# Performance work log

Hardware: AMD Instinct MI355X
Metric: run time of the kernel (lower is better)

Reference implementation:

```python
import jax, jax.numpy as jnp
import numpy as np

NEG = -1e9
THRESH = 0.97


def _gat(x, emask, W, al, ar, b):
    # x: [B,N,Fin], emask: [B,N,N] bool (src,dst), W: [Fin,H*D], al/ar: [H,D], b: [H*D]
    B, N, _ = x.shape
    H, D = al.shape
    feat = (x @ W).reshape(B, N, H, D)
    el = jnp.einsum('bnhd,hd->bnh', feat, al)
    er = jnp.einsum('bnhd,hd->bnh', feat, ar)
    # DGL GATConv: e = leaky_relu(el[src] + er[dst]); edge softmax over incoming edges of dst
    e = jax.nn.leaky_relu(el[:, :, None, :] + er[:, None, :, :], 0.2)  # [B,src,dst,H]
    e = jnp.where(emask[..., None], e, NEG)
    a = jnp.where(emask[..., None], jax.nn.softmax(e, axis=1), 0.0)  # softmax over src
    rst = jnp.einsum('bsdh,bshf->bdhf', a, feat).reshape(B, N, H * D)
    return jax.nn.elu(rst + b)


def _sem_attention(z, nmask, W1, b1, W2):
    # z: [B,N,M,Dz]; masked mean over all valid nodes of the batched graph (== DGL batch semantics)
    p = jnp.tanh(z @ W1 + b1) @ W2  # [B,N,M,1]
    w = (p * nmask[:, :, None, None]).sum(axis=(0, 1)) / nmask.sum()  # [M,1]
    beta = jax.nn.softmax(w, axis=0)  # [M,1]
    return (beta[None, None] * z).sum(axis=2)  # [B,N,Dz]


def _han_layer(h, emasks, nmask, fc, al, ar, b, sW1, sb1, sW2):
    M = fc.shape[0]
    embs = [_gat(h, emasks[m], fc[m], al[m], ar[m], b[m]) for m in range(M)]
    z = jnp.stack(embs, axis=2)  # [B,N,M,H*D]
    return _sem_attention(z, nmask, sW1, sb1, sW2)


def setup_inputs() -> dict:
    key = jax.random.key(0)
    ks = jax.random.split(key, 24)
    B, M, N, Fin = 4, 5, 1000, 64
    H, D = 4, 64
    HD = H * D  # 256
    SH = 128    # semantic attention hidden
    OUT = 5
    s = 0.1
    inp = {
        'x': jax.random.normal(ks[0], (B, M, N, Fin), dtype=jnp.float32),
        'adj': jax.random.uniform(ks[1], (B, M, N, N), dtype=jnp.float32),
        'node_nums': jax.random.randint(ks[2], (B,), 0, N),
        # layer 1 (in = Fin)
        'gat_fc1': jax.random.normal(ks[3], (M, Fin, HD), dtype=jnp.float32) * s,
        'gat_al1': jax.random.normal(ks[4], (M, H, D), dtype=jnp.float32) * s,
        'gat_ar1': jax.random.normal(ks[5], (M, H, D), dtype=jnp.float32) * s,
        'gat_b1': jnp.zeros((M, HD), dtype=jnp.float32),
        'sem_W1_1': jax.random.normal(ks[6], (HD, SH), dtype=jnp.float32) * s,
        'sem_b1_1': jnp.zeros((SH,), dtype=jnp.float32),
        'sem_W2_1': jax.random.normal(ks[7], (SH, 1), dtype=jnp.float32) * s,
        # layer 2 (in = HD)
        'gat_fc2': jax.random.normal(ks[8], (M, HD, HD), dtype=jnp.float32) * s,
        'gat_al2': jax.random.normal(ks[9], (M, H, D), dtype=jnp.float32) * s,
        'gat_ar2': jax.random.normal(ks[10], (M, H, D), dtype=jnp.float32) * s,
        'gat_b2': jnp.zeros((M, HD), dtype=jnp.float32),
        'sem_W1_2': jax.random.normal(ks[11], (HD, SH), dtype=jnp.float32) * s,
        'sem_b1_2': jnp.zeros((SH,), dtype=jnp.float32),
        'sem_W2_2': jax.random.normal(ks[12], (SH, 1), dtype=jnp.float32) * s,
        # prediction head
        'pred_W': jax.random.normal(ks[13], (HD, OUT), dtype=jnp.float32) * s,
        'pred_b': jnp.zeros((OUT,), dtype=jnp.float32),
    }
    return inp


def reference(x, adj, node_nums, gat_fc1, gat_al1, gat_ar1, gat_b1,
              sem_W1_1, sem_b1_1, sem_W2_1,
              gat_fc2, gat_al2, gat_ar2, gat_b2,
              sem_W1_2, sem_b1_2, sem_W2_2,
              pred_W, pred_b):
    B, M, N, Fin = x.shape
    h = x[:, 0]  # original cat-then-[0]: only channel-0 features are used
    nmask = (jnp.arange(N)[None, :] < node_nums[:, None]).astype(x.dtype)  # [B,N]
    pair = (nmask[:, :, None] * nmask[:, None, :]) > 0  # [B,N,N]
    emasks = [(adj[:, m] > THRESH) & pair for m in range(M)]
    h = _han_layer(h, emasks, nmask, gat_fc1, gat_al1, gat_ar1, gat_b1,
                   sem_W1_1, sem_b1_1, sem_W2_1)
    h = _han_layer(h, emasks, nmask, gat_fc2, gat_al2, gat_ar2, gat_b2,
                   sem_W1_2, sem_b1_2, sem_W2_2)
    logits = (h @ pred_W + pred_b) * nmask[:, :, None]  # scatter into padded [B,N,OUT]
    return logits
```

## Files before the change

kernel.cpp:

```cpp
#include <hip/hip_runtime.h>
#include <hip/hip_bf16.h>

#define B_ 4
#define M_ 5
#define N_ 1000
#define FIN 64
#define H_ 4
#define D_ 64
#define HD 256
#define SH 128
#define OUTD 5
#define NW 16
#define THRESH_ 0.97f

typedef unsigned short u16;
typedef u16 us8 __attribute__((ext_vector_type(8)));
typedef short s16x8 __attribute__((ext_vector_type(8)));
typedef float f32x4 __attribute__((ext_vector_type(4)));

__device__ inline u16 bf16_bits(float v) {
  __hip_bfloat16 h = __float2bfloat16(v);
  return *reinterpret_cast<u16*>(&h);
}
__device__ inline float bf16_val(u16 b) {
  __hip_bfloat16 h;
  *reinterpret_cast<u16*>(&h) = b;
  return __bfloat162float(h);
}
__device__ inline float b2f(u16 u) {
  union { unsigned int i; float f; } c;
  c.i = ((unsigned int)u) << 16;
  return c.f;
}
__device__ inline void split2(float v, u16& h, u16& l) {
  h = bf16_bits(v);
  l = bf16_bits(v - bf16_val(h));
}
__device__ inline void beta_from_sums(const float* __restrict__ psum,
                                      const int* __restrict__ node_nums,
                                      float* bb) {
  float tot = (float)(node_nums[0] + node_nums[1] + node_nums[2] + node_nums[3]);
  float w[M_], mx = -1e30f;
#pragma unroll
  for (int m = 0; m < M_; ++m) {
    w[m] = psum[m] / tot;
    mx = fmaxf(mx, w[m]);
  }
  float s = 0.f;
#pragma unroll
  for (int m = 0; m < M_; ++m) {
    w[m] = __expf(w[m] - mx);
    s += w[m];
  }
  float inv = 1.f / s;
#pragma unroll
  for (int m = 0; m < M_; ++m) bb[m] = w[m] * inv;
}

__device__ void splitT_body(const float* __restrict__ s, u16* __restrict__ hiT,
                            u16* __restrict__ loT, int K, int N, int k0, int n0,
                            char* smem) {
  float(*tile)[33] = (float(*)[33])smem;
  int tid = threadIdx.x;
  int kl = tid >> 3, nq = (tid & 7) * 4;
  *(float4*)&tile[kl][nq] = *(const float4*)(s + (size_t)(k0 + kl) * N + n0 + nq);
  __syncthreads();
  int nl = tid >> 3, kq = (tid & 7) * 4;
  ushort4 h, l;
  split2(tile[kq + 0][nl], h.x, l.x);
  split2(tile[kq + 1][nl], h.y, l.y);
  split2(tile[kq + 2][nl], h.z, l.z);
  split2(tile[kq + 3][nl], h.w, l.w);
  size_t o = (size_t)(n0 + nl) * K + k0 + kq;
  *(ushort4*)(hiT + o) = h;
  *(ushort4*)(loT + o) = l;
}

__global__ __launch_bounds__(256) void prep_all(
    const float* __restrict__ adj, const int* __restrict__ node_nums,
    unsigned long long* __restrict__ maskW,
    const float* __restrict__ fc1, u16* __restrict__ fc1Th, u16* __restrict__ fc1Tl,
    const float* __restrict__ fc2, u16* __restrict__ fc2Th, u16* __restrict__ fc2Tl,
    const float* __restrict__ sW1_1, u16* __restrict__ sW1Th1, u16* __restrict__ sW1Tl1,
    const float* __restrict__ sW1_2, u16* __restrict__ sW1Th2, u16* __restrict__ sW1Tl2) {
  __shared__ __align__(16) char smem[4608];
  int bi = blockIdx.x;
  int tid = threadIdx.x;
  if (bi < 5120) {
    int bx = bi & 15, by = (bi >> 4) & 15, bm = bi >> 8;
    int b = bm / M_;
    int s0 = bx * 64, d0 = by * 64;
    int nn = node_nums[b];
    unsigned char(*tile)[65] = (unsigned char(*)[65])smem;
    const float* arow = adj + (size_t)bm * N_ * N_;
#pragma unroll
    for (int k = 0; k < 16; ++k) {
      int idx = k * 256 + tid;
      int sl = idx >> 6, dl = idx & 63;
      int s = s0 + sl, d = d0 + dl;
      unsigned char v = 0;
      if (s < nn && d < nn && s < N_ && d < N_)
        v = (arow[(size_t)s * N_ + d] > THRESH_) ? 1 : 0;
      tile[sl][dl] = v;
    }
    __syncthreads();
    int w = tid >> 6, lane = tid & 63;
#pragma unroll
    for (int j = 0; j < 16; ++j) {
      int dl = w * 16 + j;
      bool act = tile[lane][dl] != 0;
      unsigned long long word = __ballot(act);
      int d = d0 + dl;
      if (lane == 0 && d < N_)
        maskW[((size_t)bm * N_ + d) * NW + bx] = word;
    }
    return;
  }
  bi -= 5120;
  if (bi < 80) {
    int kx = bi % 2, ny = (bi / 2) % 8, z = bi / 16;
    splitT_body(fc1 + (size_t)z * FIN * HD, fc1Th + (size_t)z * HD * FIN,
                fc1Tl + (size_t)z * HD * FIN, FIN, HD, kx * 32, ny * 32, smem);
    return;
  }
  bi -= 80;
  if (bi < 320) {
    int kx = bi % 8, ny = (bi / 8) % 8, z = bi / 64;
    splitT_body(fc2 + (size_t)z * HD * HD, fc2Th + (size_t)z * HD * HD,
                fc2Tl + (size_t)z * HD * HD, HD, HD, kx * 32, ny * 32, smem);
    return;
  }
  bi -= 320;
  if (bi < 32) {
    int kx = bi % 8, ny = bi / 8;
    splitT_body(sW1_1, sW1Th1, sW1Tl1, HD, SH, kx * 32, ny * 32, smem);
    return;
  }
  bi -= 32;
  {
    int kx = bi % 8, ny = bi / 8;
    splitT_body(sW1_2, sW1Th2, sW1Tl2, HD, SH, kx * 32, ny * 32, smem);
  }
}

__global__ __launch_bounds__(256) void gemm_mfma3(
    const float* __restrict__ A, int Mz, size_t aZ,
    const u16* __restrict__ Bh, const u16* __restrict__ Bl, size_t bZ,
    u16* __restrict__ Cbf, size_t cZ,
    int Mrows, int K, int Nc,
    const float* __restrict__ al, const float* __restrict__ ar,
    float* __restrict__ el, float* __restrict__ er) {
  __shared__ u16 sAh[64][40], sAl[64][40], sBh[64][40], sBl[64][40];
  __shared__ float elbuf[64][2], erbuf[64][2];
  int z = blockIdx.z;
  int b = z / Mz, m = z % Mz;
  const float* Ab = A + (size_t)b * aZ;
  const u16* Bhb = Bh + (size_t)m * bZ;
  const u16* Blb = Bl + (size_t)m * bZ;
  u16* Cfb = Cbf + (size_t)z * cZ;
  int row0 = blockIdx.x * 64, col0 = blockIdx.y * 64;
  int tid = threadIdx.x;
  int arow = tid >> 2, akq = (tid & 3) * 8;
  int wid = tid >> 6, lane = tid & 63;
  int wr = (wid >> 1) * 32, wc = (wid & 1) * 32;
  int lrow = lane & 15, kseg = (lane >> 4) * 8;
  f32x4 zero4 = {0.f, 0.f, 0.f, 0.f};
  f32x4 acc[2][2];
  acc[0][0] = zero4; acc[0][1] = zero4; acc[1][0] = zero4; acc[1][1] = zero4;
  for (int k0 = 0; k0 < K; k0 += 32) {
    float4 a0 = make_float4(0.f, 0.f, 0.f, 0.f), a1 = a0;
    int gr = row0 + arow;
    if (gr < Mrows) {
      const float* ap = Ab + (size_t)gr * K + k0 + akq;
      a0 = *(const float4*)ap;
      a1 = *(const float4*)(ap + 4);
    }
    us8 hv, lv;
    {
      u16 th, tl;
      split2(a0.x, th, tl); hv[0] = th; lv[0] = tl;
      split2(a0.y, th, tl); hv[1] = th; lv[1] = tl;
      split2(a0.z, th, tl); hv[2] = th; lv[2] = tl;
      split2(a0.w, th, tl); hv[3] = th; lv[3] = tl;
      split2(a1.x, th, tl); hv[4] = th; lv[4] = tl;
      split2(a1.y, th, tl); hv[5] = th; lv[5] = tl;
      split2(a1.z, th, tl); hv[6] = th; lv[6] = tl;
      split2(a1.w, th, tl); hv[7] = th; lv[7] = tl;
    }
    *(us8*)&sAh[arow][akq] = hv;
    *(us8*)&sAl[arow][akq] = lv;
    us8 bv = *(const us8*)(Bhb + (size_t)(col0 + arow) * K + k0 + akq);
    us8 blv = *(const us8*)(Blb + (size_t)(col0 + arow) * K + k0 + akq);
    *(us8*)&sBh[arow][akq] = bv;
    *(us8*)&sBl[arow][akq] = blv;
    __syncthreads();
    s16x8 aH[2], aL[2], bH[2], bL[2];
#pragma unroll
    for (int i = 0; i < 2; ++i) {
      aH[i] = *(const s16x8*)&sAh[wr + 16 * i + lrow][kseg];
      aL[i] = *(const s16x8*)&sAl[wr + 16 * i + lrow][kseg];
      bH[i] = *(const s16x8*)&sBh[wc + 16 * i + lrow][kseg];
      bL[i] = *(const s16x8*)&sBl[wc + 16 * i + lrow][kseg];
    }
#pragma unroll
    for (int i = 0; i < 2; ++i)
#pragma unroll
      for (int j = 0; j < 2; ++j) {
        acc[i][j] = __builtin_amdgcn_mfma_f32_16x16x32_bf16(aH[i], bH[j], acc[i][j], 0, 0, 0);
        acc[i][j] = __builtin_amdgcn_mfma_f32_16x16x32_bf16(aH[i], bL[j], acc[i][j], 0, 0, 0);
        acc[i][j] = __builtin_amdgcn_mfma_f32_16x16x32_bf16(aL[i], bH[j], acc[i][j], 0, 0, 0);
      }
    __syncthreads();
  }
#pragma unroll
  for (int i = 0; i < 2; ++i)
#pragma unroll
    for (int j = 0; j < 2; ++j) {
      int ccol = col0 + wc + 16 * j + lrow;
#pragma unroll
      for (int r = 0; r < 4; ++r) {
        int crow = row0 + wr + 16 * i + (lane >> 4) * 4 + r;
        if (crow < Mrows)
          Cfb[(size_t)crow * Nc + ccol] = bf16_bits(acc[i][j][r]);
      }
    }
  float alv0 = al[m * HD + col0 + wc + lrow];
  float alv1 = al[m * HD + col0 + wc + 16 + lrow];
  float arv0 = ar[m * HD + col0 + wc + lrow];
  float arv1 = ar[m * HD + col0 + wc + 16 + lrow];
#pragma unroll
  for (int i = 0; i < 2; ++i)
#pragma unroll
    for (int r = 0; r < 4; ++r) {
      float pl = acc[i][0][r] * alv0 + acc[i][1][r] * alv1;
      float pr = acc[i][0][r] * arv0 + acc[i][1][r] * arv1;
#pragma unroll
      for (int s = 1; s < 16; s <<= 1) {
        pl += __shfl_xor(pl, s, 64);
        pr += __shfl_xor(pr, s, 64);
      }
      if (lrow == 0) {
        int rl = wr + 16 * i + (lane >> 4) * 4 + r;
        elbuf[rl][wc >> 5] = pl;
        erbuf[rl][wc >> 5] = pr;
      }
    }
  __syncthreads();
  if (tid < 64) {
    int grow = row0 + tid;
    if (grow < Mrows) {
      int h = col0 >> 6;
      size_t bmN = (size_t)(b * M_ + m) * N_;
      el[(bmN + grow) * H_ + h] = elbuf[tid][0] + elbuf[tid][1];
      er[(bmN + grow) * H_ + h] = erbuf[tid][0] + erbuf[tid][1];
    }
  }
}

__global__ __launch_bounds__(256) void gat_agg(
    const unsigned long long* __restrict__ maskW, const u16* __restrict__ featbf,
    const float* __restrict__ el, const float* __restrict__ er,
    const float* __restrict__ gb, u16* __restrict__ zbh,
    float* __restrict__ psum) {
  int wid = threadIdx.x >> 6, lane = threadIdx.x & 63;
  const int NWGQ = (B_ * M_ * N_ / 4) / 8;
  int orig = blockIdx.x;
  if (orig == 0 && threadIdx.x < 8) psum[threadIdx.x] = 0.f;
  int bid = (orig & 7) * NWGQ + (orig >> 3);
  int gw = bid * 4 + wid;
  int d = gw % N_, bm = gw / N_;
  int m = bm % M_, b = bm / M_;
  __shared__ u16 slist_all[4][1032];
  u16* slist = slist_all[wid];

  const unsigned long long* mrow = maskW + ((size_t)bm * N_ + d) * NW;
  int cnt = 0;
#pragma unroll
  for (int q = 0; q < NW / 2; ++q) {
    ulonglong2 wp = *(const ulonglong2*)(mrow + q * 2);
    unsigned long long w0 = wp.x, w1 = wp.y;
    if (w0) {
      if ((w0 >> lane) & 1ull) {
        int pos = cnt + (int)__popcll(w0 & ((1ull << lane) - 1ull));
        slist[pos] = (u16)(q * 128 + lane);
      }
      cnt += (int)__popcll(w0);
    }
    if (w1) {
      if ((w1 >> lane) & 1ull) {
        int pos = cnt + (int)__popcll(w1 & ((1ull << lane) - 1ull));
        slist[pos] = (u16)(q * 128 + 64 + lane);
      }
      cnt += (int)__popcll(w1);
    }
  }

  int h = lane >> 4;
  float4 bias4 = *(const float4*)(gb + m * HD + lane * 4);
  size_t zoff = ((size_t)(b * N_ + d) * M_ + m) * HD + lane * 4;
  float4 o;
  if (cnt == 0) {
    o.x = bias4.x > 0.f ? bias4.x : (__expf(bias4.x) - 1.f);
    o.y = bias4.y > 0.f ? bias4.y : (__expf(bias4.y) - 1.f);
    o.z = bias4.z > 0.f ? bias4.z : (__expf(bias4.z) - 1.f);
    o.w = bias4.w > 0.f ? bias4.w : (__expf(bias4.w) - 1.f);
  } else {
    if (lane < 4) slist[cnt + lane] = slist[0];
    size_t bmN = (size_t)bm * N_;
    float erv = er[(bmN + d) * H_ + h];
    const float* elb = el + bmN * H_;
    const u16* fbb = featbf + bmN * HD;
    int lane4 = lane * 4;
    float den0 = 0.f, den1 = 0.f, den2 = 0.f, den3 = 0.f;
    f32x4 A0 = {0.f, 0.f, 0.f, 0.f}, A1 = A0, A2 = A0, A3 = A0;
    for (int i = 0; i < cnt; i += 4) {
      ushort4 s4 = *(const ushort4*)&slist[i];
      float e0 = elb[(size_t)s4.x * H_ + h];
      float e1 = elb[(size_t)s4.y * H_ + h];
      float e2 = elb[(size_t)s4.z * H_ + h];
      float e3 = elb[(size_t)s4.w * H_ + h];
      ushort4 g0 = *(const ushort4*)(fbb + (size_t)s4.x * HD + lane4);
      ushort4 g1 = *(const ushort4*)(fbb + (size_t)s4.y * HD + lane4);
      ushort4 g2 = *(const ushort4*)(fbb + (size_t)s4.z * HD + lane4);
      ushort4 g3 = *(const ushort4*)(fbb + (size_t)s4.w * HD + lane4);
      float v0 = e0 + erv; v0 = v0 > 0.f ? v0 : 0.2f * v0;
      float v1 = e1 + erv; v1 = v1 > 0.f ? v1 : 0.2f * v1;
      float v2 = e2 + erv; v2 = v2 > 0.f ? v2 : 0.2f * v2;
      float v3 = e3 + erv; v3 = v3 > 0.f ? v3 : 0.2f * v3;
      float w0 = __expf(v0);
      float w1 = __expf(v1) * ((i + 1 < cnt) ? 1.f : 0.f);
      float w2 = __expf(v2) * ((i + 2 < cnt) ? 1.f : 0.f);
      float w3 = __expf(v3) * ((i + 3 < cnt) ? 1.f : 0.f);
      f32x4 f0 = {b2f(g0.x), b2f(g0.y), b2f(g0.z), b2f(g0.w)};
      f32x4 f1 = {b2f(g1.x), b2f(g1.y), b2f(g1.z), b2f(g1.w)};
      f32x4 f2 = {b2f(g2.x), b2f(g2.y), b2f(g2.z), b2f(g2.w)};
      f32x4 f3 = {b2f(g3.x), b2f(g3.y), b2f(g3.z), b2f(g3.w)};
      den0 += w0; den1 += w1; den2 += w2; den3 += w3;
      A0 += w0 * f0; A1 += w1 * f1; A2 += w2 * f2; A3 += w3 * f3;
    }
    float den = (den0 + den1) + (den2 + den3);
    f32x4 A = (A0 + A1) + (A2 + A3);
    float inv = 1.f / den;
    o.x = A[0] * inv + bias4.x;
    o.y = A[1] * inv + bias4.y;
    o.z = A[2] * inv + bias4.z;
    o.w = A[3] * inv + bias4.w;
    o.x = o.x > 0.f ? o.x : (__expf(o.x) - 1.f);
    o.y = o.y > 0.f ? o.y : (__expf(o.y) - 1.f);
    o.z = o.z > 0.f ? o.z : (__expf(o.z) - 1.f);
    o.w = o.w > 0.f ? o.w : (__expf(o.w) - 1.f);
  }
  ushort4 hh;
  hh.x = bf16_bits(o.x);
  hh.y = bf16_bits(o.y);
  hh.z = bf16_bits(o.z);
  hh.w = bf16_bits(o.w);
  *(ushort4*)(zbh + zoff) = hh;
}

__global__ __launch_bounds__(256) void gemm_sem(
    const u16* __restrict__ Ah, const u16* __restrict__ Bh,
    const float* __restrict__ bias, const float* __restrict__ W2,
    float* __restrict__ psum, const int* __restrict__ node_nums, int Mrows) {
  __shared__ u16 sA[64][40], sB[64][40];
  __shared__ float redm[M_];
  int row0 = blockIdx.x * 64, col0 = blockIdx.y * 64;
  int tid = threadIdx.x;
  int arow = tid >> 2, akq = (tid & 3) * 8;
  int wid = tid >> 6, lane = tid & 63;
  int wr = (wid >> 1) * 32, wc = (wid & 1) * 32;
  int lrow = lane & 15, kseg = (lane >> 4) * 8;
  if (tid < M_) redm[tid] = 0.f;
  f32x4 zero4 = {0.f, 0.f, 0.f, 0.f};
  f32x4 acc[2][2];
  acc[0][0] = zero4; acc[0][1] = zero4; acc[1][0] = zero4; acc[1][1] = zero4;
  for (int k0 = 0; k0 < HD; k0 += 32) {
    us8 av = {0, 0, 0, 0, 0, 0, 0, 0};
    int gr = row0 + arow;
    if (gr < Mrows) av = *(const us8*)(Ah + (size_t)gr * HD + k0 + akq);
    *(us8*)&sA[arow][akq] = av;
    us8 bv = *(const us8*)(Bh + (size_t)(col0 + arow) * HD + k0 + akq);
    *(us8*)&sB[arow][akq] = bv;
    __syncthreads();
    s16x8 aH[2], bH[2];
#pragma unroll
    for (int i = 0; i < 2; ++i) {
      aH[i] = *(const s16x8*)&sA[wr + 16 * i + lrow][kseg];
      bH[i] = *(const s16x8*)&sB[wc + 16 * i + lrow][kseg];
    }
#pragma unroll
    for (int i = 0; i < 2; ++i)
#pragma unroll
      for (int j = 0; j < 2; ++j)
        acc[i][j] = __builtin_amdgcn_mfma_f32_16x16x32_bf16(aH[i], bH[j], acc[i][j], 0, 0, 0);
    __syncthreads();
  }
  int nn0 = node_nums[0], nn1 = node_nums[1], nn2 = node_nums[2], nn3 = node_nums[3];
#pragma unroll
  for (int i = 0; i < 2; ++i) {
#pragma unroll
    for (int r = 0; r < 4; ++r) {
      float part = 0.f;
#pragma unroll
      for (int j = 0; j < 2; ++j) {
        int ccol = col0 + wc + 16 * j + lrow;
        float v = tanhf(acc[i][j][r] + bias[ccol]);
        part += v * W2[ccol];
      }
#pragma unroll
      for (int s = 1; s < 16; s <<= 1) part += __shfl_xor(part, s, 64);
      int crow = row0 + wr + 16 * i + (lane >> 4) * 4 + r;
      if (lrow == 0 && crow < Mrows) {
        int m = crow % M_;
        int bn = crow / M_;
        int bb = bn / N_, n = bn % N_;
        int nn = (bb == 0) ? nn0 : (bb == 1) ? nn1 : (bb == 2) ? nn2 : nn3;
        if (n < nn) atomicAdd(&redm[m], part);
      }
    }
  }
  __syncthreads();
  if (tid < M_) atomicAdd(&psum[tid], redm[tid]);
}

__global__ __launch_bounds__(256) void sem_combine(const u16* __restrict__ zbh,
                                                   const float* __restrict__ psum,
                                                   const int* __restrict__ node_nums,
                                                   float* __restrict__ hout) {
  float bb[M_];
  beta_from_sums(psum, node_nums, bb);
  int q = blockIdx.x * 256 + threadIdx.x;
  int hd4 = (q & 63) * 4;
  int bn = q >> 6;
  const u16* zr = zbh + (size_t)bn * M_ * HD + hd4;
  f32x4 acc = {0.f, 0.f, 0.f, 0.f};
#pragma unroll
  for (int m = 0; m < M_; ++m) {
    ushort4 g = *(const ushort4*)(zr + m * HD);
    f32x4 f = {b2f(g.x), b2f(g.y), b2f(g.z), b2f(g.w)};
    acc += bb[m] * f;
  }
  *(f32x4*)(hout + (size_t)bn * HD + hd4) = acc;
}

__global__ __launch_bounds__(256) void sem_combine_pred(
    const u16* __restrict__ zbh, const float* __restrict__ psum,
    const int* __restrict__ node_nums, const float* __restrict__ W,
    const float* __restrict__ bias, float* __restrict__ out) {
  float bb[M_];
  beta_from_sums(psum, node_nums, bb);
  int row = blockIdx.x * 4 + (threadIdx.x >> 6);
  int lane = threadIdx.x & 63;
  int b = row / N_, n = row % N_;
  const u16* zr = zbh + (size_t)row * M_ * HD + lane * 4;
  float hx = 0.f, hy = 0.f, hz = 0.f, hw = 0.f;
#pragma unroll
  for (int m = 0; m < M_; ++m) {
    ushort4 g = *(const ushort4*)(zr + m * HD);
    hx += bb[m] * b2f(g.x);
    hy += bb[m] * b2f(g.y);
    hz += bb[m] * b2f(g.z);
    hw += bb[m] * b2f(g.w);
  }
  int k = lane * 4;
  float res[OUTD];
#pragma unroll
  for (int o = 0; o < OUTD; ++o) {
    float v = hx * W[(k + 0) * OUTD + o] + hy * W[(k + 1) * OUTD + o] +
              hz * W[(k + 2) * OUTD + o] + hw * W[(k + 3) * OUTD + o];
#pragma unroll
    for (int s = 1; s < 64; s <<= 1) v += __shfl_xor(v, s, 64);
    res[o] = v;
  }
  if (lane == 0) {
    float nm = (n < node_nums[b]) ? 1.f : 0.f;
#pragma unroll
    for (int o = 0; o < OUTD; ++o)
      out[(size_t)row * OUTD + o] = (res[o] + bias[o]) * nm;
  }
}

extern "C" void kernel_launch(void* const* d_in, const int* in_sizes, int n_in,
                              void* d_out, int out_size, void* d_ws, size_t ws_size,
                              hipStream_t stream) {
  const float* x = (const float*)d_in[0];
  const float* adj = (const float*)d_in[1];
  const int* node_nums = (const int*)d_in[2];
  const float* fc1 = (const float*)d_in[3];
  const float* al1 = (const float*)d_in[4];
  const float* ar1 = (const float*)d_in[5];
  const float* gb1 = (const float*)d_in[6];
  const float* sW1_1 = (const float*)d_in[7];
  const float* sb1_1 = (const float*)d_in[8];
  const float* sW2_1 = (const float*)d_in[9];
  const float* fc2 = (const float*)d_in[10];
  const float* al2 = (const float*)d_in[11];
  const float* ar2 = (const float*)d_in[12];
  const float* gb2 = (const float*)d_in[13];
  const float* sW1_2 = (const float*)d_in[14];
  const float* sb1_2 = (const float*)d_in[15];
  const float* sW2_2 = (const float*)d_in[16];
  const float* predW = (const float*)d_in[17];
  const float* predb = (const float*)d_in[18];
  float* out = (float*)d_out;

  char* ws = (char*)d_ws;
  size_t off = 0;
  unsigned long long* maskW = (unsigned long long*)(ws + off);
  off += (size_t)B_ * M_ * N_ * NW * 8;
  u16* featbf = (u16*)(ws + off); off += (size_t)B_ * M_ * N_ * HD * 2;
  float* el = (float*)(ws + off); off += (size_t)B_ * M_ * N_ * H_ * 4;
  float* er = (float*)(ws + off); off += (size_t)B_ * M_ * N_ * H_ * 4;
  u16* zbh = (u16*)(ws + off); off += (size_t)B_ * N_ * M_ * HD * 2;
  float* h1 = (float*)(ws + off); off += (size_t)B_ * N_ * HD * 4;
  float* psum = (float*)(ws + off); off += 64;
  u16* fc1Th = (u16*)(ws + off); off += (size_t)M_ * HD * FIN * 2;
  u16* fc1Tl = (u16*)(ws + off); off += (size_t)M_ * HD * FIN * 2;
  u16* fc2Th = (u16*)(ws + off); off += (size_t)M_ * HD * HD * 2;
  u16* fc2Tl = (u16*)(ws + off); off += (size_t)M_ * HD * HD * 2;
  u16* sW1Th1 = (u16*)(ws + off); off += (size_t)SH * HD * 2;
  u16* sW1Tl1 = (u16*)(ws + off); off += (size_t)SH * HD * 2;
  u16* sW1Th2 = (u16*)(ws + off); off += (size_t)SH * HD * 2;
  u16* sW1Tl2 = (u16*)(ws + off); off += (size_t)SH * HD * 2;

  const int ROWS = B_ * N_ * M_;
  const int PREP_BLOCKS = 5120 + 80 + 320 + 32 + 32;

  prep_all<<<dim3(PREP_BLOCKS), 256, 0, stream>>>(
      adj, node_nums, maskW, fc1, fc1Th, fc1Tl, fc2, fc2Th, fc2Tl,
      sW1_1, sW1Th1, sW1Tl1, sW1_2, sW1Th2, sW1Tl2);

  gemm_mfma3<<<dim3(16, HD / 64, B_ * M_), 256, 0, stream>>>(
      x, M_, (size_t)M_ * N_ * FIN, fc1Th, fc1Tl, (size_t)HD * FIN,
      featbf, (size_t)N_ * HD, N_, FIN, HD, al1, ar1, el, er);
  gat_agg<<<dim3(ROWS / 4), 256, 0, stream>>>(maskW, featbf, el, er, gb1, zbh, psum);
  gemm_sem<<<dim3((ROWS + 63) / 64, SH / 64), 256, 0, stream>>>(
      zbh, sW1Th1, sb1_1, sW2_1, psum, node_nums, ROWS);
  sem_combine<<<dim3(B_ * N_ * HD / 1024), 256, 0, stream>>>(zbh, psum, node_nums, h1);

  gemm_mfma3<<<dim3(16, HD / 64, B_ * M_), 256, 0, stream>>>(
      h1, M_, (size_t)N_ * HD, fc2Th, fc2Tl, (size_t)HD * HD,
      featbf, (size_t)N_ * HD, N_, HD, HD, al2, ar2, el, er);
  gat_agg<<<dim3(ROWS / 4), 256, 0, stream>>>(maskW, featbf, el, er, gb2, zbh, psum);
  gemm_sem<<<dim3((ROWS + 63) / 64, SH / 64), 256, 0, stream>>>(
      zbh, sW1Th2, sb1_2, sW2_2, psum, node_nums, ROWS);
  sem_combine_pred<<<dim3(B_ * N_ / 4), 256, 0, stream>>>(
      zbh, psum, node_nums, predW, predb, out);
}
```

Measured before the change: 164.6 us.

## Fuse semantic combine into layer-2 GEMM and process two destinations per wave

Drops the separate sem_combine kernel and the h1 buffer. The layer-2 feature GEMM now builds its A operand on the fly as the beta-weighted sum of the five bf16 metapath embeddings. gat_agg is restructured so each wave aggregates two destination nodes (d and d+500) together with interleaved gathers, halving the grid and adding memory-level parallelism. In exchange, the GEMM redoes the beta-weighted sum for every column block, and the paired destinations pad to the longer of their two neighbor lists.

New measurement: 192.0 us. 16.6% more time.

```diff
diff --git a/kernel.cpp b/kernel.cpp
--- a/kernel.cpp
+++ b/kernel.cpp
@@ -145,6 +145,8 @@
 
 __global__ __launch_bounds__(256) void gemm_mfma3(
     const float* __restrict__ A, int Mz, size_t aZ,
+    const u16* __restrict__ zsrc, const float* __restrict__ psum,
+    const int* __restrict__ node_nums,
     const u16* __restrict__ Bh, const u16* __restrict__ Bl, size_t bZ,
     u16* __restrict__ Cbf, size_t cZ,
     int Mrows, int K, int Nc,
@@ -154,7 +156,7 @@
   __shared__ float elbuf[64][2], erbuf[64][2];
   int z = blockIdx.z;
   int b = z / Mz, m = z % Mz;
-  const float* Ab = A + (size_t)b * aZ;
+  const float* Ab = A ? (A + (size_t)b * aZ) : nullptr;
   const u16* Bhb = Bh + (size_t)m * bZ;
   const u16* Blb = Bl + (size_t)m * bZ;
   u16* Cfb = Cbf + (size_t)z * cZ;
@@ -164,28 +166,41 @@
   int wid = tid >> 6, lane = tid & 63;
   int wr = (wid >> 1) * 32, wc = (wid & 1) * 32;
   int lrow = lane & 15, kseg = (lane >> 4) * 8;
+  float bbw[M_];
+  if (zsrc) beta_from_sums(psum, node_nums, bbw);
   f32x4 zero4 = {0.f, 0.f, 0.f, 0.f};
   f32x4 acc[2][2];
   acc[0][0] = zero4; acc[0][1] = zero4; acc[1][0] = zero4; acc[1][1] = zero4;
   for (int k0 = 0; k0 < K; k0 += 32) {
-    float4 a0 = make_float4(0.f, 0.f, 0.f, 0.f), a1 = a0;
+    float a8[8];
+#pragma unroll
+    for (int e = 0; e < 8; ++e) a8[e] = 0.f;
     int gr = row0 + arow;
     if (gr < Mrows) {
-      const float* ap = Ab + (size_t)gr * K + k0 + akq;
-      a0 = *(const float4*)ap;
-      a1 = *(const float4*)(ap + 4);
+      if (zsrc) {
+        const u16* zr = zsrc + ((size_t)(b * N_ + gr) * M_) * HD + k0 + akq;
+#pragma unroll
+        for (int mm = 0; mm < M_; ++mm) {
+          us8 g = *(const us8*)(zr + mm * HD);
+#pragma unroll
+          for (int e = 0; e < 8; ++e) a8[e] += bbw[mm] * b2f(g[e]);
+        }
+      } else {
+        const float* ap = Ab + (size_t)gr * K + k0 + akq;
+        float4 q0 = *(const float4*)ap;
+        float4 q1 = *(const float4*)(ap + 4);
+        a8[0] = q0.x; a8[1] = q0.y; a8[2] = q0.z; a8[3] = q0.w;
+        a8[4] = q1.x; a8[5] = q1.y; a8[6] = q1.z; a8[7] = q1.w;
+      }
     }
     us8 hv, lv;
     {
       u16 th, tl;
-      split2(a0.x, th, tl); hv[0] = th; lv[0] = tl;
-      split2(a0.y, th, tl); hv[1] = th; lv[1] = tl;
-      split2(a0.z, th, tl); hv[2] = th; lv[2] = tl;
-      split2(a0.w, th, tl); hv[3] = th; lv[3] = tl;
-      split2(a1.x, th, tl); hv[4] = th; lv[4] = tl;
-      split2(a1.y, th, tl); hv[5] = th; lv[5] = tl;
-      split2(a1.z, th, tl); hv[6] = th; lv[6] = tl;
-      split2(a1.w, th, tl); hv[7] = th; lv[7] = tl;
+#pragma unroll
+      for (int e = 0; e < 8; ++e) {
+        split2(a8[e], th, tl);
+        hv[e] = th; lv[e] = tl;
+      }
     }
     *(us8*)&sAh[arow][akq] = hv;
     *(us8*)&sAl[arow][akq] = lv;
@@ -263,99 +278,143 @@
     const float* __restrict__ gb, u16* __restrict__ zbh,
     float* __restrict__ psum) {
   int wid = threadIdx.x >> 6, lane = threadIdx.x & 63;
-  const int NWGQ = (B_ * M_ * N_ / 4) / 8;
+  const int NWG = (B_ * M_ * 500) / 4;
   int orig = blockIdx.x;
   if (orig == 0 && threadIdx.x < 8) psum[threadIdx.x] = 0.f;
-  int bid = (orig & 7) * NWGQ + (orig >> 3);
-  int gw = bid * 4 + wid;
-  int d = gw % N_, bm = gw / N_;
+  int q = NWG >> 3, r = NWG & 7;
+  int xcd = orig & 7, ii = orig >> 3;
+  int bid = (xcd < r ? xcd * (q + 1) : r * (q + 1) + (xcd - r) * q) + ii;
+  int ghw = bid * 4 + wid;
+  int bm = ghw / 500;
+  int db = ghw % 500;
+  int d0 = db, d1 = db + 500;
   int m = bm % M_, b = bm / M_;
-  __shared__ u16 slist_all[4][1032];
-  u16* slist = slist_all[wid];
-
-  const unsigned long long* mrow = maskW + ((size_t)bm * N_ + d) * NW;
-  int cnt = 0;
-#pragma unroll
-  for (int q = 0; q < NW / 2; ++q) {
-    ulonglong2 wp = *(const ulonglong2*)(mrow + q * 2);
-    unsigned long long w0 = wp.x, w1 = wp.y;
-    if (w0) {
-      if ((w0 >> lane) & 1ull) {
-        int pos = cnt + (int)__popcll(w0 & ((1ull << lane) - 1ull));
-        slist[pos] = (u16)(q * 128 + lane);
-      }
-      cnt += (int)__popcll(w0);
-    }
-    if (w1) {
-      if ((w1 >> lane) & 1ull) {
-        int pos = cnt + (int)__popcll(w1 & ((1ull << lane) - 1ull));
-        slist[pos] = (u16)(q * 128 + 64 + lane);
-      }
-      cnt += (int)__popcll(w1);
-    }
-  }
+  __shared__ u16 slist_all[4][2][1040];
+  u16* sl0 = slist_all[wid][0];
+  u16* sl1 = slist_all[wid][1];
+  if (lane < 4) { sl0[lane] = 0; sl1[lane] = 0; }
+
+  const unsigned long long* mr0 = maskW + ((size_t)bm * N_ + d0) * NW;
+  const unsigned long long* mr1 = maskW + ((size_t)bm * N_ + d1) * NW;
+  unsigned long long lm = (1ull << lane) - 1ull;
+  int c0 = 0, c1 = 0;
+#pragma unroll
+  for (int qq = 0; qq < NW / 2; ++qq) {
+    ulonglong2 wp0 = *(const ulonglong2*)(mr0 + qq * 2);
+    ulonglong2 wp1 = *(const ulonglong2*)(mr1 + qq * 2);
+    unsigned long long w00 = wp0.x, w01 = wp0.y, w10 = wp1.x, w11 = wp1.y;
+    if (w00) {
+      if ((w00 >> lane) & 1ull) sl0[c0 + (int)__popcll(w00 & lm)] = (u16)(qq * 128 + lane);
+      c0 += (int)__popcll(w00);
+    }
+    if (w01) {
+      if ((w01 >> lane) & 1ull) sl0[c0 + (int)__popcll(w01 & lm)] = (u16)(qq * 128 + 64 + lane);
+      c0 += (int)__popcll(w01);
+    }
+    if (w10) {
+      if ((w10 >> lane) & 1ull) sl1[c1 + (int)__popcll(w10 & lm)] = (u16)(qq * 128 + lane);
+      c1 += (int)__popcll(w10);
+    }
+    if (w11) {
+      if ((w11 >> lane) & 1ull) sl1[c1 + (int)__popcll(w11 & lm)] = (u16)(qq * 128 + 64 + lane);
+      c1 += (int)__popcll(w11);
+    }
+  }
+  int cmax = ((c0 > c1 ? c0 : c1) + 3) & ~3;
+  u16 p0 = sl0[0], p1 = sl1[0];
+  for (int t = c0 + lane; t < cmax; t += 64) sl0[t] = p0;
+  for (int t = c1 + lane; t < cmax; t += 64) sl1[t] = p1;
 
   int h = lane >> 4;
-  float4 bias4 = *(const float4*)(gb + m * HD + lane * 4);
-  size_t zoff = ((size_t)(b * N_ + d) * M_ + m) * HD + lane * 4;
-  float4 o;
-  if (cnt == 0) {
-    o.x = bias4.x > 0.f ? bias4.x : (__expf(bias4.x) - 1.f);
-    o.y = bias4.y > 0.f ? bias4.y : (__expf(bias4.y) - 1.f);
-    o.z = bias4.z > 0.f ? bias4.z : (__expf(bias4.z) - 1.f);
-    o.w = bias4.w > 0.f ? bias4.w : (__expf(bias4.w) - 1.f);
-  } else {
-    if (lane < 4) slist[cnt + lane] = slist[0];
-    size_t bmN = (size_t)bm * N_;
-    float erv = er[(bmN + d) * H_ + h];
-    const float* elb = el + bmN * H_;
-    const u16* fbb = featbf + bmN * HD;
-    int lane4 = lane * 4;
-    float den0 = 0.f, den1 = 0.f, den2 = 0.f, den3 = 0.f;
-    f32x4 A0 = {0.f, 0.f, 0.f, 0.f}, A1 = A0, A2 = A0, A3 = A0;
-    for (int i = 0; i < cnt; i += 4) {
-      ushort4 s4 = *(const ushort4*)&slist[i];
-      float e0 = elb[(size_t)s4.x * H_ + h];
-      float e1 = elb[(size_t)s4.y * H_ + h];
-      float e2 = elb[(size_t)s4.z * H_ + h];
-      float e3 = elb[(size_t)s4.w * H_ + h];
-      ushort4 g0 = *(const ushort4*)(fbb + (size_t)s4.x * HD + lane4);
-      ushort4 g1 = *(const ushort4*)(fbb + (size_t)s4.y * HD + lane4);
-      ushort4 g2 = *(const ushort4*)(fbb + (size_t)s4.z * HD + lane4);
-      ushort4 g3 = *(const ushort4*)(fbb + (size_t)s4.w * HD + lane4);
-      float v0 = e0 + erv; v0 = v0 > 0.f ? v0 : 0.2f * v0;
-      float v1 = e1 + erv; v1 = v1 > 0.f ? v1 : 0.2f * v1;
-      float v2 = e2 + erv; v2 = v2 > 0.f ? v2 : 0.2f * v2;
-      float v3 = e3 + erv; v3 = v3 > 0.f ? v3 : 0.2f * v3;
-      float w0 = __expf(v0);
-      float w1 = __expf(v1) * ((i + 1 < cnt) ? 1.f : 0.f);
-      float w2 = __expf(v2) * ((i + 2 < cnt) ? 1.f : 0.f);
-      float w3 = __expf(v3) * ((i + 3 < cnt) ? 1.f : 0.f);
-      f32x4 f0 = {b2f(g0.x), b2f(g0.y), b2f(g0.z), b2f(g0.w)};
-      f32x4 f1 = {b2f(g1.x), b2f(g1.y), b2f(g1.z), b2f(g1.w)};
-      f32x4 f2 = {b2f(g2.x), b2f(g2.y), b2f(g2.z), b2f(g2.w)};
-      f32x4 f3 = {b2f(g3.x), b2f(g3.y), b2f(g3.z), b2f(g3.w)};
-      den0 += w0; den1 += w1; den2 += w2; den3 += w3;
-      A0 += w0 * f0; A1 += w1 * f1; A2 += w2 * f2; A3 += w3 * f3;
-    }
-    float den = (den0 + den1) + (den2 + den3);
-    f32x4 A = (A0 + A1) + (A2 + A3);
-    float inv = 1.f / den;
-    o.x = A[0] * inv + bias4.x;
-    o.y = A[1] * inv + bias4.y;
-    o.z = A[2] * inv + bias4.z;
-    o.w = A[3] * inv + bias4.w;
-    o.x = o.x > 0.f ? o.x : (__expf(o.x) - 1.f);
-    o.y = o.y > 0.f ? o.y : (__expf(o.y) - 1.f);
-    o.z = o.z > 0.f ? o.z : (__expf(o.z) - 1.f);
-    o.w = o.w > 0.f ? o.w : (__expf(o.w) - 1.f);
-  }
-  ushort4 hh;
-  hh.x = bf16_bits(o.x);
-  hh.y = bf16_bits(o.y);
-  hh.z = bf16_bits(o.z);
-  hh.w = bf16_bits(o.w);
-  *(ushort4*)(zbh + zoff) = hh;
+  int lane4 = lane * 4;
+  float4 bias4 = *(const float4*)(gb + m * HD + lane4);
+  size_t bmN = (size_t)bm * N_;
+  float erv0 = er[(bmN + d0) * H_ + h];
+  float erv1 = er[(bmN + d1) * H_ + h];
+  const float* elb = el + bmN * H_;
+  const u16* fbb = featbf + bmN * HD;
+
+  float dA0 = 0.f, dA1 = 0.f, dA2 = 0.f, dA3 = 0.f;
+  float dB0 = 0.f, dB1 = 0.f, dB2 = 0.f, dB3 = 0.f;
+  f32x4 zz = {0.f, 0.f, 0.f, 0.f};
+  f32x4 AA0 = zz, AA1 = zz, AA2 = zz, AA3 = zz;
+  f32x4 BB0 = zz, BB1 = zz, BB2 = zz, BB3 = zz;
+  for (int i = 0; i < cmax; i += 4) {
+    ushort4 sa = *(const ushort4*)&sl0[i];
+    ushort4 sb = *(const ushort4*)&sl1[i];
+    float ea0 = elb[(size_t)sa.x * H_ + h];
+    float ea1 = elb[(size_t)sa.y * H_ + h];
+    float ea2 = elb[(size_t)sa.z * H_ + h];
+    float ea3 = elb[(size_t)sa.w * H_ + h];
+    float eb0 = elb[(size_t)sb.x * H_ + h];
+    float eb1 = elb[(size_t)sb.y * H_ + h];
+    float eb2 = elb[(size_t)sb.z * H_ + h];
+    float eb3 = elb[(size_t)sb.w * H_ + h];
+    ushort4 ga0 = *(const ushort4*)(fbb + (size_t)sa.x * HD + lane4);
+    ushort4 ga1 = *(const ushort4*)(fbb + (size_t)sa.y * HD + lane4);
+    ushort4 ga2 = *(const ushort4*)(fbb + (size_t)sa.z * HD + lane4);
+    ushort4 ga3 = *(const ushort4*)(fbb + (size_t)sa.w * HD + lane4);
+    ushort4 gb0 = *(const ushort4*)(fbb + (size_t)sb.x * HD + lane4);
+    ushort4 gb1 = *(const ushort4*)(fbb + (size_t)sb.y * HD + lane4);
+    ushort4 gb2 = *(const ushort4*)(fbb + (size_t)sb.z * HD + lane4);
+    ushort4 gb3 = *(const ushort4*)(fbb + (size_t)sb.w * HD + lane4);
+    float va0 = ea0 + erv0; va0 = va0 > 0.f ? va0 : 0.2f * va0;
+    float va1 = ea1 + erv0; va1 = va1 > 0.f ? va1 : 0.2f * va1;
+    float va2 = ea2 + erv0; va2 = va2 > 0.f ? va2 : 0.2f * va2;
+    float va3 = ea3 + erv0; va3 = va3 > 0.f ? va3 : 0.2f * va3;
+    float vb0 = eb0 + erv1; vb0 = vb0 > 0.f ? vb0 : 0.2f * vb0;
+    float vb1 = eb1 + erv1; vb1 = vb1 > 0.f ? vb1 : 0.2f * vb1;
+    float vb2 = eb2 + erv1; vb2 = vb2 > 0.f ? vb2 : 0.2f * vb2;
+    float vb3 = eb3 + erv1; vb3 = vb3 > 0.f ? vb3 : 0.2f * vb3;
+    float wa0 = __expf(va0) * ((i + 0 < c0) ? 1.f : 0.f);
+    float wa1 = __expf(va1) * ((i + 1 < c0) ? 1.f : 0.f);
+    float wa2 = __expf(va2) * ((i + 2 < c0) ? 1.f : 0.f);
+    float wa3 = __expf(va3) * ((i + 3 < c0) ? 1.f : 0.f);
+    float wb0 = __expf(vb0) * ((i + 0 < c1) ? 1.f : 0.f);
+    float wb1 = __expf(vb1) * ((i + 1 < c1) ? 1.f : 0.f);
+    float wb2 = __expf(vb2) * ((i + 2 < c1) ? 1.f : 0.f);
+    float wb3 = __expf(vb3) * ((i + 3 < c1) ? 1.f : 0.f);
+    f32x4 fa0 = {b2f(ga0.x), b2f(ga0.y), b2f(ga0.z), b2f(ga0.w)};
+    f32x4 fa1 = {b2f(ga1.x), b2f(ga1.y), b2f(ga1.z), b2f(ga1.w)};
+    f32x4 fa2 = {b2f(ga2.x), b2f(ga2.y), b2f(ga2.z), b2f(ga2.w)};
+    f32x4 fa3 = {b2f(ga3.x), b2f(ga3.y), b2f(ga3.z), b2f(ga3.w)};
+    f32x4 fb0 = {b2f(gb0.x), b2f(gb0.y), b2f(gb0.z), b2f(gb0.w)};
+    f32x4 fb1 = {b2f(gb1.x), b2f(gb1.y), b2f(gb1.z), b2f(gb1.w)};
+    f32x4 fb2 = {b2f(gb2.x), b2f(gb2.y), b2f(gb2.z), b2f(gb2.w)};
+    f32x4 fb3 = {b2f(gb3.x), b2f(gb3.y), b2f(gb3.z), b2f(gb3.w)};
+    dA0 += wa0; dA1 += wa1; dA2 += wa2; dA3 += wa3;
+    dB0 += wb0; dB1 += wb1; dB2 += wb2; dB3 += wb3;
+    AA0 += wa0 * fa0; AA1 += wa1 * fa1; AA2 += wa2 * fa2; AA3 += wa3 * fa3;
+    BB0 += wb0 * fb0; BB1 += wb1 * fb1; BB2 += wb2 * fb2; BB3 += wb3 * fb3;
+  }
+  float denA = (dA0 + dA1) + (dA2 + dA3);
+  float denB = (dB0 + dB1) + (dB2 + dB3);
+  f32x4 SA = (AA0 + AA1) + (AA2 + AA3);
+  f32x4 SB = (BB0 + BB1) + (BB2 + BB3);
+  float invA = (c0 > 0) ? 1.f / denA : 0.f;
+  float invB = (c1 > 0) ? 1.f / denB : 0.f;
+  {
+    f32x4 o = SA * invA;
+    o[0] += bias4.x; o[1] += bias4.y; o[2] += bias4.z; o[3] += bias4.w;
+#pragma unroll
+    for (int e = 0; e < 4; ++e) o[e] = o[e] > 0.f ? o[e] : (__expf(o[e]) - 1.f);
+    ushort4 hh;
+    hh.x = bf16_bits(o[0]); hh.y = bf16_bits(o[1]);
+    hh.z = bf16_bits(o[2]); hh.w = bf16_bits(o[3]);
+    size_t zoff = ((size_t)(b * N_ + d0) * M_ + m) * HD + lane4;
+    *(ushort4*)(zbh + zoff) = hh;
+  }
+  {
+    f32x4 o = SB * invB;
+    o[0] += bias4.x; o[1] += bias4.y; o[2] += bias4.z; o[3] += bias4.w;
+#pragma unroll
+    for (int e = 0; e < 4; ++e) o[e] = o[e] > 0.f ? o[e] : (__expf(o[e]) - 1.f);
+    ushort4 hh;
+    hh.x = bf16_bits(o[0]); hh.y = bf16_bits(o[1]);
+    hh.z = bf16_bits(o[2]); hh.w = bf16_bits(o[3]);
+    size_t zoff = ((size_t)(b * N_ + d1) * M_ + m) * HD + lane4;
+    *(ushort4*)(zbh + zoff) = hh;
+  }
 }
 
 __global__ __launch_bounds__(256) void gemm_sem(
@@ -423,26 +482,6 @@
   if (tid < M_) atomicAdd(&psum[tid], redm[tid]);
 }
 
-__global__ __launch_bounds__(256) void sem_combine(const u16* __restrict__ zbh,
-                                                   const float* __restrict__ psum,
-                                                   const int* __restrict__ node_nums,
-                                                   float* __restrict__ hout) {
-  float bb[M_];
-  beta_from_sums(psum, node_nums, bb);
-  int q = blockIdx.x * 256 + threadIdx.x;
-  int hd4 = (q & 63) * 4;
-  int bn = q >> 6;
-  const u16* zr = zbh + (size_t)bn * M_ * HD + hd4;
-  f32x4 acc = {0.f, 0.f, 0.f, 0.f};
-#pragma unroll
-  for (int m = 0; m < M_; ++m) {
-    ushort4 g = *(const ushort4*)(zr + m * HD);
-    f32x4 f = {b2f(g.x), b2f(g.y), b2f(g.z), b2f(g.w)};
-    acc += bb[m] * f;
-  }
-  *(f32x4*)(hout + (size_t)bn * HD + hd4) = acc;
-}
-
 __global__ __launch_bounds__(256) void sem_combine_pred(
     const u16* __restrict__ zbh, const float* __restrict__ psum,
     const int* __restrict__ node_nums, const float* __restrict__ W,
@@ -512,7 +551,6 @@
   float* el = (float*)(ws + off); off += (size_t)B_ * M_ * N_ * H_ * 4;
   float* er = (float*)(ws + off); off += (size_t)B_ * M_ * N_ * H_ * 4;
   u16* zbh = (u16*)(ws + off); off += (size_t)B_ * N_ * M_ * HD * 2;
-  float* h1 = (float*)(ws + off); off += (size_t)B_ * N_ * HD * 4;
   float* psum = (float*)(ws + off); off += 64;
   u16* fc1Th = (u16*)(ws + off); off += (size_t)M_ * HD * FIN * 2;
   u16* fc1Tl = (u16*)(ws + off); off += (size_t)M_ * HD * FIN * 2;
@@ -531,17 +569,18 @@
       sW1_1, sW1Th1, sW1Tl1, sW1_2, sW1Th2, sW1Tl2);
 
   gemm_mfma3<<<dim3(16, HD / 64, B_ * M_), 256, 0, stream>>>(
-      x, M_, (size_t)M_ * N_ * FIN, fc1Th, fc1Tl, (size_t)HD * FIN,
+      x, M_, (size_t)M_ * N_ * FIN, nullptr, nullptr, node_nums,
+      fc1Th, fc1Tl, (size_t)HD * FIN,
       featbf, (size_t)N_ * HD, N_, FIN, HD, al1, ar1, el, er);
-  gat_agg<<<dim3(ROWS / 4), 256, 0, stream>>>(maskW, featbf, el, er, gb1, zbh, psum);
+  gat_agg<<<dim3(ROWS / 8), 256, 0, stream>>>(maskW, featbf, el, er, gb1, zbh, psum);
   gemm_sem<<<dim3((ROWS + 63) / 64, SH / 64), 256, 0, stream>>>(
       zbh, sW1Th1, sb1_1, sW2_1, psum, node_nums, ROWS);
-  sem_combine<<<dim3(B_ * N_ * HD / 1024), 256, 0, stream>>>(zbh, psum, node_nums, h1);
 
   gemm_mfma3<<<dim3(16, HD / 64, B_ * M_), 256, 0, stream>>>(
-      h1, M_, (size_t)N_ * HD, fc2Th, fc2Tl, (size_t)HD * HD,
+      nullptr, M_, 0, zbh, psum, node_nums,
+      fc2Th, fc2Tl, (size_t)HD * HD,
       featbf, (size_t)N_ * HD, N_, HD, HD, al2, ar2, el, er);
-  gat_agg<<<dim3(ROWS / 4), 256, 0, stream>>>(maskW, featbf, el, er, gb2, zbh, psum);
+  gat_agg<<<dim3(ROWS / 8), 256, 0, stream>>>(maskW, featbf, el, er, gb2, zbh, psum);
   gemm_sem<<<dim3((ROWS + 63) / 64, SH / 64), 256, 0, stream>>>(
       zbh, sW1Th2, sb1_2, sW2_2, psum, node_nums, ROWS);
   sem_combine_pred<<<dim3(B_ * N_ / 4), 256, 0, stream>>>(
```
